# Kernel tuning notes

Measured on AMD Instinct MI355X. Metric: run time of the kernel, lower is better.

Reference implementation:

```python
import jax, jax.numpy as jnp
import numpy as np

EPSILON = 0.05
MAX_ITER = 50
ALPHA = 6.0
THRESHOLD = 0.25
SCALE = 0.02  # keeps OT costs near THRESHOLD so the gate is not saturated


def setup_inputs() -> dict:
    key = jax.random.key(0)
    k1, k2 = jax.random.split(key)
    B, E, D, P = 8192, 8, 512, 32
    tokens = jax.random.normal(k1, (B, E, D), dtype=jnp.float32) * SCALE
    prototypes = jax.random.normal(k2, (E, P, D), dtype=jnp.float32) * SCALE
    return {"tokens": tokens, "prototypes": prototypes, "full_index": 0}


def _sinkhorn_log(cost, epsilon, max_iter):
    # cost: [..., n_source, n_target]; batched log-domain Sinkhorn, fixed iterations
    ns, nt = cost.shape[-2], cost.shape[-1]
    log_mu = jnp.full(cost.shape[:-1], -float(np.log(ns)), dtype=cost.dtype)
    log_nu = jnp.full(cost.shape[:-2] + (nt,), -float(np.log(nt)), dtype=cost.dtype)
    log_k = -cost / epsilon

    def step(carry, _):
        log_u, log_v = carry
        log_u = log_mu - jax.scipy.special.logsumexp(log_k + log_v[..., None, :], axis=-1)
        log_v = log_nu - jax.scipy.special.logsumexp(log_k + log_u[..., :, None], axis=-2)
        return (log_u, log_v), None

    (log_u, log_v), _ = jax.lax.scan(
        step, (jnp.zeros_like(log_mu), jnp.zeros_like(log_nu)), None, length=max_iter
    )
    return jnp.exp(log_k + log_u[..., :, None] + log_v[..., None, :])


def reference(tokens, prototypes, full_index):
    # tokens: [B, E, D], prototypes: [E, P, D]
    B, E, D = tokens.shape
    anchor = tokens[:, full_index, :]                                   # [B, D]
    source = jnp.stack(
        [tokens, jnp.broadcast_to(anchor[:, None, :], tokens.shape)], axis=2
    )                                                                   # [B, E, 2, D]
    # squared euclidean cdist: ||s||^2 - 2 s.p + ||p||^2
    s2 = jnp.sum(source * source, axis=-1)                              # [B, E, 2]
    p2 = jnp.sum(prototypes * prototypes, axis=-1)                      # [E, P]
    cross = jnp.einsum('besd,epd->besp', source, prototypes)            # [B, E, 2, P]
    cost = jnp.maximum(s2[..., None] - 2.0 * cross + p2[None, :, None, :], 0.0)
    transport = _sinkhorn_log(cost, EPSILON, MAX_ITER)                  # [B, E, 2, P]
    ot_cost = jnp.sum(transport * cost, axis=(-1, -2))                  # [B, E]
    validity = jax.nn.sigmoid(-ALPHA * (ot_cost - THRESHOLD))[..., None]  # [B, E, 1]
    # the full_index expert always passes with validity 1 and zero cost
    is_full = jnp.arange(E) == full_index                               # [E]
    ot_cost = jnp.where(is_full[None, :], 0.0, ot_cost)
    validity = jnp.where(is_full[None, :, None], 1.0, validity)
    return validity, ot_cost
```

## Files before the change

### kernel.cpp

```cpp
#include <hip/hip_runtime.h>
#include <hip/hip_bf16.h>


#define EXP2F(x) __builtin_amdgcn_exp2f(x)
#define LOG2F(x) __builtin_amdgcn_logf(x)
#define RCPF(x)  __builtin_amdgcn_rcpf(x)

typedef __bf16 bf16x8 __attribute__((ext_vector_type(8)));
typedef float  f32x4  __attribute__((ext_vector_type(4)));

#define BDIM 8192
#define EDIM 8
#define DDIM 512
#define PDIM 32
#define BPB  128
#define MROWS 256
#define NTHR 256
#define ASTRIDE 72
#define BSTRIDE 536
#define CSTRIDE 36
#define C_SCALE 28.853900817779268f
#define LOG2E   1.4426950408889634f

__device__ __forceinline__ void store_bf16x4(__bf16* dst, float4 v) {
  ushort4 t;
  t.x = __builtin_bit_cast(unsigned short, (__bf16)v.x);
  t.y = __builtin_bit_cast(unsigned short, (__bf16)v.y);
  t.z = __builtin_bit_cast(unsigned short, (__bf16)v.z);
  t.w = __builtin_bit_cast(unsigned short, (__bf16)v.w);
  *(ushort4*)dst = t;
}

__global__ void proto_norms_kernel(const float* __restrict__ protos,
                                   float* __restrict__ pn) {
  int e = blockIdx.x;
  int p = threadIdx.x >> 3;
  int j = threadIdx.x & 7;
  const float4* row = (const float4*)(protos + ((size_t)e * PDIM + p) * DDIM);
  float s = 0.f;
  #pragma unroll
  for (int k = 0; k < 16; ++k) {
    float4 v = row[j + 8 * k];
    s += v.x * v.x + v.y * v.y + v.z * v.z + v.w * v.w;
  }
  s += __shfl_xor(s, 1);
  s += __shfl_xor(s, 2);
  s += __shfl_xor(s, 4);
  if (j == 0) pn[e * PDIM + p] = s;
}

__global__ __launch_bounds__(NTHR, 2)
void ot_noise_gate_kernel(const float* __restrict__ tokens,
                          const float* __restrict__ protos,
                          const float* __restrict__ pn,
                          const int*   __restrict__ fullIndexPtr,
                          float*       __restrict__ out) {
  const int fi    = fullIndexPtr[0];
  const int e     = blockIdx.x & (EDIM - 1);
  const int chunk = blockIdx.x >> 3;
  const int b0    = chunk * BPB;
  float* outVal = out;
  float* outOt  = out + BDIM * EDIM;

  if (e == fi) {
    int t = threadIdx.x;
    if (t < BPB) {
      int b = b0 + t;
      outVal[b * EDIM + e] = 1.0f;
      outOt [b * EDIM + e] = 0.0f;
    }
    return;
  }

  __shared__ __align__(16) unsigned char sACraw[MROWS * ASTRIDE * 2];
  __shared__ __align__(16) __bf16 sB[PDIM * BSTRIDE];
  __shared__ float sNorm[MROWS];
  __bf16* sA = (__bf16*)sACraw;
  float*  sC = (float*)sACraw;

  const int t    = threadIdx.x;
  const int l    = t & 63;
  const int w    = t >> 6;
  const int fr   = l & 15;
  const int oct  = l >> 4;

  {
    const float4* pG4 = (const float4*)(protos + (size_t)e * PDIM * DDIM);
    #pragma unroll
    for (int it = 0; it < 16; ++it) {
      int idx = it * NTHR + t;
      float4 v = pG4[idx];
      store_bf16x4(&sB[(idx >> 7) * BSTRIDE + (idx & 127) * 4], v);
    }
  }

  const int g = t >> 4;
  const int j = t & 15;
  const float4* tokB = (const float4*)(tokens + ((size_t)(b0 + g) * EDIM + e)  * DDIM);
  const float4* ancB = (const float4*)(tokens + ((size_t)(b0 + g) * EDIM + fi) * DDIM);
  const int rowStrF4 = 16 * EDIM * DDIM / 4;

  float ss[16];
  #pragma unroll
  for (int r = 0; r < 16; ++r) ss[r] = 0.f;

  f32x4 acc[4][2];
  #pragma unroll
  for (int mt = 0; mt < 4; ++mt)
    #pragma unroll
    for (int nt = 0; nt < 2; ++nt)
      acc[mt][nt] = (f32x4){0.f, 0.f, 0.f, 0.f};

  for (int kc = 0; kc < 8; ++kc) {
    #pragma unroll
    for (int it = 0; it < 8; ++it) {
      float4 v = tokB[it * rowStrF4 + kc * 16 + j];
      ss[it] += v.x * v.x + v.y * v.y + v.z * v.z + v.w * v.w;
      store_bf16x4(&sA[(it * 16 + g) * ASTRIDE + j * 4], v);
    }
    #pragma unroll
    for (int it = 0; it < 8; ++it) {
      float4 v = ancB[it * rowStrF4 + kc * 16 + j];
      ss[8 + it] += v.x * v.x + v.y * v.y + v.z * v.z + v.w * v.w;
      store_bf16x4(&sA[((8 + it) * 16 + g) * ASTRIDE + j * 4], v);
    }
    __syncthreads();

    #pragma unroll
    for (int ks = 0; ks < 2; ++ks) {
      bf16x8 b0f = *(const bf16x8*)&sB[(fr)      * BSTRIDE + kc * 64 + ks * 32 + oct * 8];
      bf16x8 b1f = *(const bf16x8*)&sB[(16 + fr) * BSTRIDE + kc * 64 + ks * 32 + oct * 8];
      #pragma unroll
      for (int mt = 0; mt < 4; ++mt) {
        bf16x8 af = *(const bf16x8*)&sA[(w * 64 + mt * 16 + fr) * ASTRIDE + ks * 32 + oct * 8];
        acc[mt][0] = __builtin_amdgcn_mfma_f32_16x16x32_bf16(af, b0f, acc[mt][0], 0, 0, 0);
        acc[mt][1] = __builtin_amdgcn_mfma_f32_16x16x32_bf16(af, b1f, acc[mt][1], 0, 0, 0);
      }
    }
    __syncthreads();
  }

  #pragma unroll
  for (int it = 0; it < 16; ++it) {
    float v = ss[it];
    v += __shfl_xor(v, 1);
    v += __shfl_xor(v, 2);
    v += __shfl_xor(v, 4);
    v += __shfl_xor(v, 8);
    if (j == 0) sNorm[it * 16 + g] = v;
  }
  __syncthreads();

  {
    float pp0 = pn[e * PDIM + fr];
    float pp1 = pn[e * PDIM + 16 + fr];
    #pragma unroll
    for (int mt = 0; mt < 4; ++mt)
      #pragma unroll
      for (int reg = 0; reg < 4; ++reg) {
        int row = w * 64 + mt * 16 + oct * 4 + reg;
        float nrm = sNorm[row];
        sC[row * CSTRIDE + fr]      = fmaxf(nrm - 2.f * acc[mt][0][reg] + pp0, 0.f);
        sC[row * CSTRIDE + 16 + fr] = fmaxf(nrm - 2.f * acc[mt][1][reg] + pp1, 0.f);
      }
  }
  __syncthreads();

  const int i = t >> 1;
  const int h = t & 1;
  const float4* r0 = (const float4*)&sC[i * CSTRIDE];
  const float4* r1 = (const float4*)&sC[(128 + i) * CSTRIDE];
  float c0[16], c1[16];
  #pragma unroll
  for (int r = 0; r < 4; ++r) {
    float4 a = r0[h * 4 + r];
    float4 b = r1[h * 4 + r];
    c0[4*r] = a.x; c0[4*r+1] = a.y; c0[4*r+2] = a.z; c0[4*r+3] = a.w;
    c1[4*r] = b.x; c1[4*r+1] = b.y; c1[4*r+2] = b.z; c1[4*r+3] = b.w;
  }

  float W[16], dc[16];
  float sum0 = 0.f, mA = -1e30f, mB = -1e30f;
  #pragma unroll
  for (int r = 0; r < 16; ++r) {
    float ka = -c0[r] * C_SCALE, kb = -c1[r] * C_SCALE;
    dc[r] = c1[r] - c0[r];
    sum0 += c0[r];
    mA = fmaxf(mA, ka);
    mB = fmaxf(mB, kb);
  }
  mA = fmaxf(mA, __shfl_xor(mA, 1));
  mB = fmaxf(mB, __shfl_xor(mB, 1));
  float sa = 0.f, sb = 0.f;
  #pragma unroll
  for (int r = 0; r < 16; ++r) {
    float ka = -c0[r] * C_SCALE, kb = -c1[r] * C_SCALE;
    sa += EXP2F(ka - mA);
    sb += EXP2F(kb - mB);
    W[r] = EXP2F(C_SCALE * dc[r]);
  }
  sa += __shfl_xor(sa, 1);
  sb += __shfl_xor(sb, 1);
  sum0 += __shfl_xor(sum0, 1);
  float delta = (mB + LOG2F(sb)) - (mA + LOG2F(sa));

  for (int it = 0; it < 49; ++it) {
    float s = EXP2F(delta);
    float T = 0.f;
    #pragma unroll
    for (int r = 0; r < 16; ++r)
      T += RCPF(__builtin_fmaf(W[r], s, 1.0f));
    T += __shfl_xor(T, 1);
    delta += LOG2F(T) - LOG2F(32.0f - T);
  }

  float s = EXP2F(delta), sv = 0.f;
  #pragma unroll
  for (int r = 0; r < 16; ++r)
    sv += RCPF(__builtin_fmaf(W[r], s, 1.0f)) * dc[r];
  sv += __shfl_xor(sv, 1);
  if (h == 0) {
    int b = b0 + i;
    float ot  = (sum0 + sv) * 0.03125f;
    float val = RCPF(1.0f + EXP2F(LOG2E * 6.0f * (ot - 0.25f)));
    outVal[b * EDIM + e] = val;
    outOt [b * EDIM + e] = ot;
  }
}

extern "C" void kernel_launch(void* const* d_in, const int* in_sizes, int n_in,
                              void* d_out, int out_size, void* d_ws, size_t ws_size,
                              hipStream_t stream) {
  const float* tokens = (const float*)d_in[0];
  const float* protos = (const float*)d_in[1];
  const int*   fidx   = (const int*)d_in[2];
  float* out = (float*)d_out;
  float* pn  = (float*)d_ws;

  proto_norms_kernel<<<EDIM, NTHR, 0, stream>>>(protos, pn);
  dim3 grid((BDIM / BPB) * EDIM);
  ot_noise_gate_kernel<<<grid, NTHR, 0, stream>>>(tokens, protos, pn, fidx, out);
}
```

Measured before the change: 217.7 us.

## Halve batch tile, fuse prototype norms, prefetch token rows with register double-buffering

Drops the per-block batch tile from 128 to 64 rows and raises the launch-bounds occupancy target from 2 to 3 blocks per CU. The separate prototype-norm kernel is removed, and the norms are now computed while prototypes are staged to shared memory. Token loads are reorganised so each thread pair owns one row, and the next K chunk is prefetched into registers while MFMAs run. The shared-memory layout becomes k-octet-major, and each Sinkhorn row is now split across 4 lanes instead of 2, trading more shuffles for shorter per-lane loops. The cost is that every block repeats the prototype load and conversion, with twice as many blocks.

```diff
diff --git a/kernel.cpp b/kernel.cpp
--- a/kernel.cpp
+++ b/kernel.cpp
@@ -13,46 +13,23 @@
 #define EDIM 8
 #define DDIM 512
 #define PDIM 32
-#define BPB  128
-#define MROWS 256
+#define BPB  64
+#define MROWS 128
 #define NTHR 256
-#define ASTRIDE 72
-#define BSTRIDE 536
 #define CSTRIDE 36
 #define C_SCALE 28.853900817779268f
 #define LOG2E   1.4426950408889634f
 
-__device__ __forceinline__ void store_bf16x4(__bf16* dst, float4 v) {
-  ushort4 t;
-  t.x = __builtin_bit_cast(unsigned short, (__bf16)v.x);
-  t.y = __builtin_bit_cast(unsigned short, (__bf16)v.y);
-  t.z = __builtin_bit_cast(unsigned short, (__bf16)v.z);
-  t.w = __builtin_bit_cast(unsigned short, (__bf16)v.w);
-  *(ushort4*)dst = t;
+__device__ __forceinline__ bf16x8 cvt2(float4 a, float4 b) {
+  bf16x8 r;
+  r[0] = (__bf16)a.x; r[1] = (__bf16)a.y; r[2] = (__bf16)a.z; r[3] = (__bf16)a.w;
+  r[4] = (__bf16)b.x; r[5] = (__bf16)b.y; r[6] = (__bf16)b.z; r[7] = (__bf16)b.w;
+  return r;
 }
 
-__global__ void proto_norms_kernel(const float* __restrict__ protos,
-                                   float* __restrict__ pn) {
-  int e = blockIdx.x;
-  int p = threadIdx.x >> 3;
-  int j = threadIdx.x & 7;
-  const float4* row = (const float4*)(protos + ((size_t)e * PDIM + p) * DDIM);
-  float s = 0.f;
-  #pragma unroll
-  for (int k = 0; k < 16; ++k) {
-    float4 v = row[j + 8 * k];
-    s += v.x * v.x + v.y * v.y + v.z * v.z + v.w * v.w;
-  }
-  s += __shfl_xor(s, 1);
-  s += __shfl_xor(s, 2);
-  s += __shfl_xor(s, 4);
-  if (j == 0) pn[e * PDIM + p] = s;
-}
-
-__global__ __launch_bounds__(NTHR, 2)
+__global__ __launch_bounds__(NTHR, 3)
 void ot_noise_gate_kernel(const float* __restrict__ tokens,
                           const float* __restrict__ protos,
-                          const float* __restrict__ pn,
                           const int*   __restrict__ fullIndexPtr,
                           float*       __restrict__ out) {
   const int fi    = fullIndexPtr[0];
@@ -72,154 +49,167 @@
     return;
   }
 
-  __shared__ __align__(16) unsigned char sACraw[MROWS * ASTRIDE * 2];
-  __shared__ __align__(16) __bf16 sB[PDIM * BSTRIDE];
+  __shared__ __align__(16) __bf16 sB[64 * PDIM * 8];
+  __shared__ __align__(16) unsigned char sACraw[MROWS * CSTRIDE * 4];
   __shared__ float sNorm[MROWS];
+  __shared__ float sPNp[8][33];
+  __shared__ float sPN[PDIM];
   __bf16* sA = (__bf16*)sACraw;
   float*  sC = (float*)sACraw;
 
-  const int t    = threadIdx.x;
-  const int l    = t & 63;
-  const int w    = t >> 6;
-  const int fr   = l & 15;
-  const int oct  = l >> 4;
+  const int t   = threadIdx.x;
+  const int l   = t & 63;
+  const int w   = t >> 6;
+  const int fr  = l & 15;
+  const int q4  = l >> 4;
+
+  const int row = t >> 1;
+  const int h   = t & 1;
+  const float4* rowPtr = (const float4*)(tokens +
+      ((size_t)(b0 + (row & 63)) * EDIM + ((row < 64) ? e : fi)) * DDIM);
+
+  float4 pf[8];
+  #pragma unroll
+  for (int i2 = 0; i2 < 8; ++i2) pf[i2] = rowPtr[h * 8 + i2];
 
   {
     const float4* pG4 = (const float4*)(protos + (size_t)e * PDIM * DDIM);
-    #pragma unroll
-    for (int it = 0; it < 16; ++it) {
-      int idx = it * NTHR + t;
-      float4 v = pG4[idx];
-      store_bf16x4(&sB[(idx >> 7) * BSTRIDE + (idx & 127) * 4], v);
-    }
-  }
-
-  const int g = t >> 4;
-  const int j = t & 15;
-  const float4* tokB = (const float4*)(tokens + ((size_t)(b0 + g) * EDIM + e)  * DDIM);
-  const float4* ancB = (const float4*)(tokens + ((size_t)(b0 + g) * EDIM + fi) * DDIM);
-  const int rowStrF4 = 16 * EDIM * DDIM / 4;
-
-  float ss[16];
-  #pragma unroll
-  for (int r = 0; r < 16; ++r) ss[r] = 0.f;
-
-  f32x4 acc[4][2];
-  #pragma unroll
-  for (int mt = 0; mt < 4; ++mt)
+    const int p  = t & 31;
+    const int oh = t >> 5;
+    float pnp = 0.f;
+    #pragma unroll
+    for (int pass = 0; pass < 8; ++pass) {
+      int oct = oh * 8 + pass;
+      float4 a = pG4[p * 128 + oct * 2];
+      float4 b = pG4[p * 128 + oct * 2 + 1];
+      pnp += a.x*a.x + a.y*a.y + a.z*a.z + a.w*a.w
+           + b.x*b.x + b.y*b.y + b.z*b.z + b.w*b.w;
+      *(bf16x8*)&sB[(oct * PDIM + p) * 8] = cvt2(a, b);
+    }
+    sPNp[oh][p] = pnp;
+  }
+  __syncthreads();
+  if (t < PDIM) {
+    float s = 0.f;
+    #pragma unroll
+    for (int o = 0; o < 8; ++o) s += sPNp[o][t];
+    sPN[t] = s;
+  }
+
+  f32x4 acc[2][2];
+  #pragma unroll
+  for (int mt = 0; mt < 2; ++mt)
     #pragma unroll
     for (int nt = 0; nt < 2; ++nt)
       acc[mt][nt] = (f32x4){0.f, 0.f, 0.f, 0.f};
+  float ss = 0.f;
 
   for (int kc = 0; kc < 8; ++kc) {
     #pragma unroll
-    for (int it = 0; it < 8; ++it) {
-      float4 v = tokB[it * rowStrF4 + kc * 16 + j];
-      ss[it] += v.x * v.x + v.y * v.y + v.z * v.z + v.w * v.w;
-      store_bf16x4(&sA[(it * 16 + g) * ASTRIDE + j * 4], v);
-    }
-    #pragma unroll
-    for (int it = 0; it < 8; ++it) {
-      float4 v = ancB[it * rowStrF4 + kc * 16 + j];
-      ss[8 + it] += v.x * v.x + v.y * v.y + v.z * v.z + v.w * v.w;
-      store_bf16x4(&sA[((8 + it) * 16 + g) * ASTRIDE + j * 4], v);
+    for (int ii = 0; ii < 4; ++ii) {
+      float4 a = pf[2 * ii], b = pf[2 * ii + 1];
+      ss += a.x*a.x + a.y*a.y + a.z*a.z + a.w*a.w
+          + b.x*b.x + b.y*b.y + b.z*b.z + b.w*b.w;
+      *(bf16x8*)&sA[((h * 4 + ii) * MROWS + row) * 8] = cvt2(a, b);
     }
     __syncthreads();
 
+    if (kc < 7) {
+      #pragma unroll
+      for (int i2 = 0; i2 < 8; ++i2)
+        pf[i2] = rowPtr[(kc + 1) * 16 + h * 8 + i2];
+    }
+
     #pragma unroll
     for (int ks = 0; ks < 2; ++ks) {
-      bf16x8 b0f = *(const bf16x8*)&sB[(fr)      * BSTRIDE + kc * 64 + ks * 32 + oct * 8];
-      bf16x8 b1f = *(const bf16x8*)&sB[(16 + fr) * BSTRIDE + kc * 64 + ks * 32 + oct * 8];
+      bf16x8 bf0 = *(const bf16x8*)&sB[((kc * 8 + ks * 4 + q4) * PDIM + fr) * 8];
+      bf16x8 bf1 = *(const bf16x8*)&sB[((kc * 8 + ks * 4 + q4) * PDIM + 16 + fr) * 8];
       #pragma unroll
-      for (int mt = 0; mt < 4; ++mt) {
-        bf16x8 af = *(const bf16x8*)&sA[(w * 64 + mt * 16 + fr) * ASTRIDE + ks * 32 + oct * 8];
-        acc[mt][0] = __builtin_amdgcn_mfma_f32_16x16x32_bf16(af, b0f, acc[mt][0], 0, 0, 0);
-        acc[mt][1] = __builtin_amdgcn_mfma_f32_16x16x32_bf16(af, b1f, acc[mt][1], 0, 0, 0);
+      for (int mt = 0; mt < 2; ++mt) {
+        bf16x8 af = *(const bf16x8*)&sA[((ks * 4 + q4) * MROWS + w * 32 + mt * 16 + fr) * 8];
+        acc[mt][0] = __builtin_amdgcn_mfma_f32_16x16x32_bf16(af, bf0, acc[mt][0], 0, 0, 0);
+        acc[mt][1] = __builtin_amdgcn_mfma_f32_16x16x32_bf16(af, bf1, acc[mt][1], 0, 0, 0);
       }
     }
     __syncthreads();
   }
 
-  #pragma unroll
-  for (int it = 0; it < 16; ++it) {
-    float v = ss[it];
-    v += __shfl_xor(v, 1);
-    v += __shfl_xor(v, 2);
-    v += __shfl_xor(v, 4);
-    v += __shfl_xor(v, 8);
-    if (j == 0) sNorm[it * 16 + g] = v;
-  }
+  ss += __shfl_xor(ss, 1);
+  if (h == 0) sNorm[row] = ss;
   __syncthreads();
 
   {
-    float pp0 = pn[e * PDIM + fr];
-    float pp1 = pn[e * PDIM + 16 + fr];
-    #pragma unroll
-    for (int mt = 0; mt < 4; ++mt)
+    float pp0 = sPN[fr], pp1 = sPN[16 + fr];
+    #pragma unroll
+    for (int mt = 0; mt < 2; ++mt)
       #pragma unroll
       for (int reg = 0; reg < 4; ++reg) {
-        int row = w * 64 + mt * 16 + oct * 4 + reg;
-        float nrm = sNorm[row];
-        sC[row * CSTRIDE + fr]      = fmaxf(nrm - 2.f * acc[mt][0][reg] + pp0, 0.f);
-        sC[row * CSTRIDE + 16 + fr] = fmaxf(nrm - 2.f * acc[mt][1][reg] + pp1, 0.f);
+        int r2 = w * 32 + mt * 16 + q4 * 4 + reg;
+        float nrm = sNorm[r2];
+        sC[r2 * CSTRIDE + fr]      = fmaxf(nrm - 2.f * acc[mt][0][reg] + pp0, 0.f);
+        sC[r2 * CSTRIDE + 16 + fr] = fmaxf(nrm - 2.f * acc[mt][1][reg] + pp1, 0.f);
       }
   }
   __syncthreads();
 
-  const int i = t >> 1;
-  const int h = t & 1;
-  const float4* r0 = (const float4*)&sC[i * CSTRIDE];
-  const float4* r1 = (const float4*)&sC[(128 + i) * CSTRIDE];
-  float c0[16], c1[16];
-  #pragma unroll
-  for (int r = 0; r < 4; ++r) {
-    float4 a = r0[h * 4 + r];
-    float4 b = r1[h * 4 + r];
-    c0[4*r] = a.x; c0[4*r+1] = a.y; c0[4*r+2] = a.z; c0[4*r+3] = a.w;
-    c1[4*r] = b.x; c1[4*r+1] = b.y; c1[4*r+2] = b.z; c1[4*r+3] = b.w;
-  }
-
-  float W[16], dc[16];
+  const int i  = t >> 2;
+  const int q2 = t & 3;
+  float c0[8], c1[8];
+  {
+    const float4* r0 = (const float4*)&sC[i * CSTRIDE + q2 * 8];
+    const float4* r1 = (const float4*)&sC[(64 + i) * CSTRIDE + q2 * 8];
+    #pragma unroll
+    for (int r = 0; r < 2; ++r) {
+      float4 a = r0[r];
+      float4 b = r1[r];
+      c0[4*r] = a.x; c0[4*r+1] = a.y; c0[4*r+2] = a.z; c0[4*r+3] = a.w;
+      c1[4*r] = b.x; c1[4*r+1] = b.y; c1[4*r+2] = b.z; c1[4*r+3] = b.w;
+    }
+  }
+
+  float W[8], dc[8];
   float sum0 = 0.f, mA = -1e30f, mB = -1e30f;
   #pragma unroll
-  for (int r = 0; r < 16; ++r) {
+  for (int r = 0; r < 8; ++r) {
     float ka = -c0[r] * C_SCALE, kb = -c1[r] * C_SCALE;
     dc[r] = c1[r] - c0[r];
     sum0 += c0[r];
     mA = fmaxf(mA, ka);
     mB = fmaxf(mB, kb);
   }
-  mA = fmaxf(mA, __shfl_xor(mA, 1));
-  mB = fmaxf(mB, __shfl_xor(mB, 1));
+  mA = fmaxf(mA, __shfl_xor(mA, 1)); mA = fmaxf(mA, __shfl_xor(mA, 2));
+  mB = fmaxf(mB, __shfl_xor(mB, 1)); mB = fmaxf(mB, __shfl_xor(mB, 2));
   float sa = 0.f, sb = 0.f;
   #pragma unroll
-  for (int r = 0; r < 16; ++r) {
+  for (int r = 0; r < 8; ++r) {
     float ka = -c0[r] * C_SCALE, kb = -c1[r] * C_SCALE;
     sa += EXP2F(ka - mA);
     sb += EXP2F(kb - mB);
     W[r] = EXP2F(C_SCALE * dc[r]);
   }
-  sa += __shfl_xor(sa, 1);
-  sb += __shfl_xor(sb, 1);
-  sum0 += __shfl_xor(sum0, 1);
+  sa += __shfl_xor(sa, 1); sa += __shfl_xor(sa, 2);
+  sb += __shfl_xor(sb, 1); sb += __shfl_xor(sb, 2);
+  sum0 += __shfl_xor(sum0, 1); sum0 += __shfl_xor(sum0, 2);
   float delta = (mB + LOG2F(sb)) - (mA + LOG2F(sa));
 
   for (int it = 0; it < 49; ++it) {
     float s = EXP2F(delta);
     float T = 0.f;
     #pragma unroll
-    for (int r = 0; r < 16; ++r)
+    for (int r = 0; r < 8; ++r)
       T += RCPF(__builtin_fmaf(W[r], s, 1.0f));
     T += __shfl_xor(T, 1);
+    T += __shfl_xor(T, 2);
     delta += LOG2F(T) - LOG2F(32.0f - T);
   }
 
   float s = EXP2F(delta), sv = 0.f;
   #pragma unroll
-  for (int r = 0; r < 16; ++r)
+  for (int r = 0; r < 8; ++r)
     sv += RCPF(__builtin_fmaf(W[r], s, 1.0f)) * dc[r];
   sv += __shfl_xor(sv, 1);
-  if (h == 0) {
+  sv += __shfl_xor(sv, 2);
+  if (q2 == 0) {
     int b = b0 + i;
     float ot  = (sum0 + sv) * 0.03125f;
     float val = RCPF(1.0f + EXP2F(LOG2E * 6.0f * (ot - 0.25f)));
@@ -235,9 +225,7 @@
   const float* protos = (const float*)d_in[1];
   const int*   fidx   = (const int*)d_in[2];
   float* out = (float*)d_out;
-  float* pn  = (float*)d_ws;
-
-  proto_norms_kernel<<<EDIM, NTHR, 0, stream>>>(protos, pn);
+
   dim3 grid((BDIM / BPB) * EDIM);
-  ot_noise_gate_kernel<<<grid, NTHR, 0, stream>>>(tokens, protos, pn, fidx, out);
+  ot_noise_gate_kernel<<<grid, NTHR, 0, stream>>>(tokens, protos, fidx, out);
 }
```

After: 218.5 us. Within noise of the previous version (+0.4%).
